# Performance work log

Hardware: AMD Instinct MI355X
Metric: run time of the kernel (lower is better)

Reference implementation:

```python
import math
import jax, jax.numpy as jnp
import numpy as np

HIDDEN = 1024
INTER = 2048
NUM_EXPERTS = 8          # includes 1 noop slot (last column)
TOP_K = 2
CAPACITY_FACTOR = 1.0
BATCH, SEQ = 4, 4096


def setup_inputs() -> dict:
    key = jax.random.key(0)
    k_x, k_rw, k_ei, k_eo = jax.random.split(key, 4)
    x = jax.random.normal(k_x, (BATCH, SEQ, HIDDEN), dtype=jnp.float32)
    # Router: nn.Linear(hidden, num_experts) with xavier_uniform weight, zero-ish bias
    limit = math.sqrt(6.0 / (HIDDEN + NUM_EXPERTS))
    router_w = jax.random.uniform(k_rw, (NUM_EXPERTS, HIDDEN), dtype=jnp.float32,
                                  minval=-limit, maxval=limit)
    router_b = jnp.zeros((NUM_EXPERTS,), dtype=jnp.float32)
    # Expert params initialized with randn, exactly as in the torch module
    experts_inter = jax.random.normal(k_ei, (NUM_EXPERTS - 1, HIDDEN, INTER), dtype=jnp.float32)
    experts_out = jax.random.normal(k_eo, (NUM_EXPERTS - 1, INTER, HIDDEN), dtype=jnp.float32)
    return {"x": x, "router_w": router_w, "router_b": router_b,
            "experts_inter": experts_inter, "experts_out": experts_out}


def reference(x, router_w, router_b, experts_inter, experts_out):
    B, S, H = x.shape
    E = router_w.shape[0]
    N = B * S
    capacity = math.ceil(N / E * CAPACITY_FACTOR)  # static (shapes are static)

    x_flat = x.reshape(N, H)
    # Router: linear + softmax over experts
    weights = jax.nn.softmax(x_flat @ router_w.T + router_b, axis=-1)   # [N, E]

    # Top-k sparsification: keep top-k weights per token, zero the rest
    vals, idx = jax.lax.top_k(weights, TOP_K)                            # [N, k]
    topk_w = jnp.zeros_like(weights).at[jnp.arange(N)[:, None], idx].set(vals)

    # Last expert column is the no-op (identity) path
    noop_routed = x_flat * topk_w[:, -1:]                                # [N, H]

    expert_w = topk_w[:, :-1]                                            # [N, E-1]
    mask = (expert_w > 0).astype(jnp.int32)                              # [N, E-1]

    # Per-expert: sort tokens by routing mask (descending), take first `capacity`
    sorted_idx = jnp.argsort(-mask, axis=0)[:capacity]                   # [C, E-1], stable
    sorted_mask = jnp.take_along_axis(mask, sorted_idx, axis=0)          # [C, E-1]

    used_idx = (sorted_idx * sorted_mask).reshape(-1)                    # [C*(E-1)]
    toks = x_flat[used_idx] * sorted_mask.reshape(-1)[:, None].astype(x.dtype)
    toks = toks.reshape(capacity, E - 1, H)                              # [C, E-1, H]
    in_w = jnp.take_along_axis(expert_w, sorted_idx, axis=0)             # [C, E-1]

    # Grouped expert FFN: relu(x W1) W2, weighted by routing prob
    h = jax.nn.relu(jnp.einsum('ceh,ehi->cei', toks, experts_inter))     # [C, E-1, I]
    out = jnp.einsum('cei,eih->ceh', h, experts_out) * in_w[..., None]   # [C, E-1, H]

    # Scatter-add combine (masked slots contribute zeros at index 0)
    combined = jnp.zeros_like(x_flat).at[used_idx].add(out.reshape(-1, H))
    combined = combined + noop_routed
    return combined.reshape(B, S, H)
```

## Files before the change

kernel.cpp:

```cpp
#include <hip/hip_runtime.h>
#include <stdint.h>

#define HIDDEN 1024
#define INTER 2048
#define NEXP 8
#define NE 7
#define NTOK 16384
#define CAP 2048
#define GBM 128
#define GBN 128

typedef __attribute__((ext_vector_type(8))) short short8;
typedef __attribute__((ext_vector_type(4))) float f32x4;

__device__ __forceinline__ unsigned short f2bf(float f) {
  union { float f; unsigned int u; } v;
  v.f = f;
  unsigned int u = v.u;
  unsigned int r = (u + 0x7FFFu + ((u >> 16) & 1u)) >> 16;
  return (unsigned short)r;
}

typedef __attribute__((address_space(1))) const unsigned int gu32;
typedef __attribute__((address_space(3))) unsigned int lu32;
__device__ __forceinline__ void gload16(const void* g, void* l) {
  __builtin_amdgcn_global_load_lds((gu32*)g, (lu32*)l, 16, 0, 0);
}

__global__ __launch_bounds__(256) void prologue_kernel(
    const float* __restrict__ x, const float* __restrict__ rw,
    const float* __restrict__ rb, float* __restrict__ expw,
    float* __restrict__ noopw, unsigned short* __restrict__ xbf,
    float* __restrict__ out, const float* __restrict__ wi,
    unsigned short* __restrict__ wiT) {
  int bx = blockIdx.x;
  int tid = threadIdx.x;
  if (bx > NTOK / 4) {
    int i = bx - (NTOK / 4 + 1);
    int e = i >> 9;
    int rem = i & 511;
    int k0 = (rem >> 5) * 64;
    int n0 = (rem & 31) * 64;
    const float* src = wi + (size_t)e * HIDDEN * INTER;
    unsigned short* dst = wiT + (size_t)e * HIDDEN * INTER;
    __shared__ float tile[64][65];
    int nr = tid & 15, kr = tid >> 4;
#pragma unroll
    for (int ii = 0; ii < 4; ii++) {
      int k = ii * 16 + kr;
      float4 v = *(const float4*)(src + (size_t)(k0 + k) * INTER + n0 + nr * 4);
      tile[k][nr * 4 + 0] = v.x;
      tile[k][nr * 4 + 1] = v.y;
      tile[k][nr * 4 + 2] = v.z;
      tile[k][nr * 4 + 3] = v.w;
    }
    __syncthreads();
    int g = tid & 7, nb = tid >> 3;
#pragma unroll
    for (int ii = 0; ii < 2; ii++) {
      int n = ii * 32 + nb;
      short8 p;
#pragma unroll
      for (int j = 0; j < 8; j++) p[j] = (short)f2bf(tile[g * 8 + j][n]);
      *(short8*)(dst + (size_t)(n0 + n) * HIDDEN + k0 + g * 8) = p;
    }
    return;
  }
  if (bx == NTOK / 4) {
    unsigned int* z = (unsigned int*)(xbf + (size_t)NTOK * HIDDEN);
    z[tid] = 0u;
    z[tid + 256] = 0u;
    return;
  }
  int wid = tid >> 6;
  int lane = tid & 63;
  int token = bx * 4 + wid;
  const float* xr = x + (size_t)token * HIDDEN;
  float4 xv[4];
  float acc[NEXP];
#pragma unroll
  for (int e = 0; e < NEXP; e++) acc[e] = 0.f;
#pragma unroll
  for (int j = 0; j < 4; j++) {
    xv[j] = *(const float4*)(xr + j * 256 + lane * 4);
#pragma unroll
    for (int e = 0; e < NEXP; e++) {
      float4 wv = *(const float4*)(rw + e * HIDDEN + j * 256 + lane * 4);
      acc[e] = fmaf(xv[j].x, wv.x, acc[e]);
      acc[e] = fmaf(xv[j].y, wv.y, acc[e]);
      acc[e] = fmaf(xv[j].z, wv.z, acc[e]);
      acc[e] = fmaf(xv[j].w, wv.w, acc[e]);
    }
  }
#pragma unroll
  for (int e = 0; e < NEXP; e++) {
    float a = acc[e];
#pragma unroll
    for (int off = 32; off > 0; off >>= 1) a += __shfl_xor(a, off);
    acc[e] = a + rb[e];
  }
  float nwv = 0.f;
  if (lane == 0) {
    float m = acc[0];
#pragma unroll
    for (int e = 1; e < NEXP; e++) m = fmaxf(m, acc[e]);
    float w[NEXP];
    float s = 0.f;
#pragma unroll
    for (int e = 0; e < NEXP; e++) { w[e] = expf(acc[e] - m); s += w[e]; }
    float inv = 1.f / s;
#pragma unroll
    for (int e = 0; e < NEXP; e++) w[e] *= inv;
    int t1 = 0;
#pragma unroll
    for (int e = 1; e < NEXP; e++) if (w[e] > w[t1]) t1 = e;
    int t2 = (t1 == 0) ? 1 : 0;
#pragma unroll
    for (int e = 0; e < NEXP; e++) if (e != t1 && w[e] > w[t2]) t2 = e;
    nwv = (t1 == NEXP - 1) ? w[t1] : ((t2 == NEXP - 1) ? w[t2] : 0.f);
    noopw[token] = nwv;
#pragma unroll
    for (int e = 0; e < NE; e++) {
      float v = 0.f;
      if (e == t1) v = w[e];
      if (e == t2) v = w[e];
      expw[(size_t)e * NTOK + token] = v;
    }
  }
  float nw = __shfl(nwv, 0);
  float* orow = out + (size_t)token * HIDDEN;
  unsigned short* brow = xbf + (size_t)token * HIDDEN;
#pragma unroll
  for (int j = 0; j < 4; j++) {
    float4 o = xv[j];
    o.x *= nw; o.y *= nw; o.z *= nw; o.w *= nw;
    *(float4*)(orow + j * 256 + lane * 4) = o;
    ushort4 b;
    b.x = f2bf(xv[j].x); b.y = f2bf(xv[j].y);
    b.z = f2bf(xv[j].z); b.w = f2bf(xv[j].w);
    *(ushort4*)(brow + j * 256 + lane * 4) = b;
  }
}

__global__ __launch_bounds__(1024) void assign_par_kernel(
    const float* __restrict__ expw, int* __restrict__ slot_tok,
    float* __restrict__ slot_w) {
  int e = blockIdx.x;
  int tid = threadIdx.x;
  int lane = tid & 63, w = tid >> 6;
  __shared__ int wtot[16];
  const float* we = expw + (size_t)e * NTOK;
  int base = 0;
#pragma unroll 1
  for (int r = 0; r < NTOK / 1024; r++) {
    int t = r * 1024 + tid;
    float wv = we[t];
    bool flag = wv > 0.f;
    unsigned long long mask = __ballot(flag);
    int lp = __popcll(mask & ((1ull << lane) - 1ull));
    if (lane == 0) wtot[w] = __popcll(mask);
    __syncthreads();
    int pre = 0, tot = 0;
#pragma unroll
    for (int i = 0; i < 16; i++) {
      int v = wtot[i];
      pre += (i < w) ? v : 0;
      tot += v;
    }
    int pos = base + pre + lp;
    if (flag && pos < CAP) {
      slot_tok[e * CAP + pos] = t;
      slot_w[e * CAP + pos] = wv;
    }
    base += tot;
    __syncthreads();
    if (base >= CAP) break;
  }
  int cnt = base < CAP ? base : CAP;
  for (int p = cnt + tid; p < CAP; p += 1024) {
    slot_tok[e * CAP + p] = -1;
    slot_w[e * CAP + p] = 0.f;
  }
}

__global__ __launch_bounds__(256) void transpose_bf16_kernel(
    const float* __restrict__ in, unsigned short* __restrict__ outp,
    int K, int N) {
  int e = blockIdx.z;
  const float* src = in + (size_t)e * K * N;
  unsigned short* dst = outp + (size_t)e * K * N;
  int k0 = blockIdx.y * 64;
  int n0 = blockIdx.x * 64;
  __shared__ float tile[64][65];
  int tid = threadIdx.x;
  int nr = tid & 15;
  int kr = tid >> 4;
#pragma unroll
  for (int i = 0; i < 4; i++) {
    int k = i * 16 + kr;
    float4 v = *(const float4*)(src + (size_t)(k0 + k) * N + n0 + nr * 4);
    tile[k][nr * 4 + 0] = v.x;
    tile[k][nr * 4 + 1] = v.y;
    tile[k][nr * 4 + 2] = v.z;
    tile[k][nr * 4 + 3] = v.w;
  }
  __syncthreads();
  int g = tid & 7;
  int nb = tid >> 3;
#pragma unroll
  for (int i = 0; i < 2; i++) {
    int n = i * 32 + nb;
    short8 p;
#pragma unroll
    for (int j = 0; j < 8; j++) p[j] = (short)f2bf(tile[g * 8 + j][n]);
    *(short8*)(dst + (size_t)(n0 + n) * K + k0 + g * 8) = p;
  }
}

__global__ __launch_bounds__(512, 4) void gemm1_mfma_kernel(
    const unsigned short* __restrict__ xbf, const unsigned short* __restrict__ wiT,
    const int* __restrict__ slot_tok, unsigned short* __restrict__ h,
    const float* __restrict__ wo, unsigned short* __restrict__ woT) {
  __shared__ __align__(16) unsigned short smem[GBM * 64 + GBN * 64];
  unsigned short* As = smem;
  unsigned short* Bs = smem + GBM * 64;
  int tid = threadIdx.x;
  if (blockIdx.y >= 16) {
    int e = blockIdx.z;
    int k0 = (blockIdx.y - 16) * 64;
    int n0 = blockIdx.x * 64;
    const float* src = wo + (size_t)e * INTER * HIDDEN;
    unsigned short* dst = woT + (size_t)e * INTER * HIDDEN;
    float* tile = (float*)smem;
    int nr = tid & 15, kr = tid >> 4;
#pragma unroll
    for (int ii = 0; ii < 2; ii++) {
      int k = ii * 32 + kr;
      float4 v = *(const float4*)(src + (size_t)(k0 + k) * HIDDEN + n0 + nr * 4);
      tile[k * 65 + nr * 4 + 0] = v.x;
      tile[k * 65 + nr * 4 + 1] = v.y;
      tile[k * 65 + nr * 4 + 2] = v.z;
      tile[k * 65 + nr * 4 + 3] = v.w;
    }
    __syncthreads();
    int g = tid & 7, n = tid >> 3;
    short8 p;
#pragma unroll
    for (int j = 0; j < 8; j++) p[j] = (short)f2bf(tile[(g * 8 + j) * 65 + n]);
    *(short8*)(dst + (size_t)(n0 + n) * INTER + k0 + g * 8) = p;
    return;
  }
  int orig = blockIdx.x + (blockIdx.y << 4) + (blockIdx.z << 8);
  int swz = (orig & 7) * 224 + (orig >> 3);
  int bxi = swz & 15, byi = (swz >> 4) & 15, bzi = swz >> 8;
  int e = bzi;
  const unsigned short* be = wiT + (size_t)e * HIDDEN * INTER;
  unsigned short* he = h + (size_t)e * CAP * INTER;
  int bm0 = byi * GBM;
  int bn0 = bxi * GBN;
  int lane = tid & 63, w = tid >> 6;
  int wm = w >> 2, wn = w & 3;

  const unsigned short* aptr[2];
  const unsigned short* bptr[2];
#pragma unroll
  for (int c = 0; c < 2; c++) {
    int slot = c * 512 + tid;
    int r = slot >> 3;
    int gb = slot & 7;
    int g = gb ^ (r & 7);
    int tok = slot_tok[e * CAP + bm0 + r];
    int row = tok < 0 ? NTOK : tok;
    aptr[c] = xbf + (size_t)row * HIDDEN + g * 8;
    bptr[c] = be + (size_t)(bn0 + r) * HIDDEN + g * 8;
  }

  f32x4 acc[4][2];
#pragma unroll
  for (int i = 0; i < 4; i++)
#pragma unroll
    for (int j = 0; j < 2; j++) acc[i][j] = (f32x4){0.f, 0.f, 0.f, 0.f};

  for (int k0 = 0; k0 < HIDDEN; k0 += 64) {
#pragma unroll
    for (int c = 0; c < 2; c++) {
      gload16(aptr[c] + k0, As + (c * 512 + tid) * 8);
      gload16(bptr[c] + k0, Bs + (c * 512 + tid) * 8);
    }
    __syncthreads();
#pragma unroll
    for (int kk = 0; kk < 2; kk++) {
      short8 a[4], b[2];
#pragma unroll
      for (int fm = 0; fm < 4; fm++) {
        int r = wm * 64 + fm * 16 + (lane & 15);
        int gb = (kk * 4 + (lane >> 4)) ^ (r & 7);
        a[fm] = *(const short8*)&As[r * 64 + gb * 8];
      }
#pragma unroll
      for (int fn = 0; fn < 2; fn++) {
        int n = wn * 32 + fn * 16 + (lane & 15);
        int gb = (kk * 4 + (lane >> 4)) ^ (n & 7);
        b[fn] = *(const short8*)&Bs[n * 64 + gb * 8];
      }
#pragma unroll
      for (int fm = 0; fm < 4; fm++)
#pragma unroll
        for (int fn = 0; fn < 2; fn++)
          acc[fm][fn] = __builtin_amdgcn_mfma_f32_16x16x32_bf16(
              a[fm], b[fn], acc[fm][fn], 0, 0, 0);
    }
    __syncthreads();
  }
#pragma unroll
  for (int fm = 0; fm < 4; fm++)
#pragma unroll
    for (int r4 = 0; r4 < 4; r4++) {
      int m = bm0 + wm * 64 + fm * 16 + ((lane >> 4) << 2) + r4;
#pragma unroll
      for (int fn = 0; fn < 2; fn++) {
        int n = bn0 + wn * 32 + fn * 16 + (lane & 15);
        float v = acc[fm][fn][r4];
        he[(size_t)m * INTER + n] = f2bf(v > 0.f ? v : 0.f);
      }
    }
}

__global__ __launch_bounds__(512, 4) void gemm2_mfma_kernel(
    const unsigned short* __restrict__ h, const unsigned short* __restrict__ woT,
    const int* __restrict__ slot_tok, const float* __restrict__ slot_w,
    float* __restrict__ out) {
  int orig = blockIdx.x + (blockIdx.y << 3) + (blockIdx.z << 7);
  int swz = (orig & 7) * 112 + (orig >> 3);
  int bxi = swz & 7, byi = (swz >> 3) & 15, bzi = swz >> 7;
  int e = bzi;
  const unsigned short* ae = h + (size_t)e * CAP * INTER;
  const unsigned short* be = woT + (size_t)e * INTER * HIDDEN;
  int bm0 = byi * GBM;
  int bn0 = bxi * GBN;
  __shared__ __align__(16) unsigned short smem[GBM * 64 + GBN * 64];
  unsigned short* As = smem;
  unsigned short* Bs = smem + GBM * 64;
  int tid = threadIdx.x;
  int lane = tid & 63, w = tid >> 6;
  int wm = w >> 2, wn = w & 3;

  const unsigned short* aptr[2];
  const unsigned short* bptr[2];
#pragma unroll
  for (int c = 0; c < 2; c++) {
    int slot = c * 512 + tid;
    int r = slot >> 3;
    int gb = slot & 7;
    int g = gb ^ (r & 7);
    aptr[c] = ae + (size_t)(bm0 + r) * INTER + g * 8;
    bptr[c] = be + (size_t)(bn0 + r) * INTER + g * 8;
  }

  f32x4 acc[4][2];
#pragma unroll
  for (int i = 0; i < 4; i++)
#pragma unroll
    for (int j = 0; j < 2; j++) acc[i][j] = (f32x4){0.f, 0.f, 0.f, 0.f};

  for (int k0 = 0; k0 < INTER; k0 += 64) {
#pragma unroll
    for (int c = 0; c < 2; c++) {
      gload16(aptr[c] + k0, As + (c * 512 + tid) * 8);
      gload16(bptr[c] + k0, Bs + (c * 512 + tid) * 8);
    }
    __syncthreads();
#pragma unroll
    for (int kk = 0; kk < 2; kk++) {
      short8 a[4], b[2];
#pragma unroll
      for (int fm = 0; fm < 4; fm++) {
        int r = wm * 64 + fm * 16 + (lane & 15);
        int gb = (kk * 4 + (lane >> 4)) ^ (r & 7);
        a[fm] = *(const short8*)&As[r * 64 + gb * 8];
      }
#pragma unroll
      for (int fn = 0; fn < 2; fn++) {
        int n = wn * 32 + fn * 16 + (lane & 15);
        int gb = (kk * 4 + (lane >> 4)) ^ (n & 7);
        b[fn] = *(const short8*)&Bs[n * 64 + gb * 8];
      }
#pragma unroll
      for (int fm = 0; fm < 4; fm++)
#pragma unroll
        for (int fn = 0; fn < 2; fn++)
          acc[fm][fn] = __builtin_amdgcn_mfma_f32_16x16x32_bf16(
              a[fm], b[fn], acc[fm][fn], 0, 0, 0);
    }
    __syncthreads();
  }
#pragma unroll
  for (int fm = 0; fm < 4; fm++)
#pragma unroll
    for (int r4 = 0; r4 < 4; r4++) {
      int m = bm0 + wm * 64 + fm * 16 + ((lane >> 4) << 2) + r4;
      int tok = slot_tok[e * CAP + m];
      float sw = slot_w[e * CAP + m];
      if (tok >= 0) {
#pragma unroll
        for (int fn = 0; fn < 2; fn++) {
          int n = bn0 + wn * 32 + fn * 16 + (lane & 15);
          unsafeAtomicAdd(out + (size_t)tok * HIDDEN + n, acc[fm][fn][r4] * sw);
        }
      }
    }
}

extern "C" void kernel_launch(void* const* d_in, const int* in_sizes, int n_in,
                              void* d_out, int out_size, void* d_ws, size_t ws_size,
                              hipStream_t stream) {
  const float* x = (const float*)d_in[0];
  const float* rw = (const float*)d_in[1];
  const float* rb = (const float*)d_in[2];
  const float* wi = (const float*)d_in[3];
  const float* wo = (const float*)d_in[4];
  float* out = (float*)d_out;
  char* ws = (char*)d_ws;

  const size_t h_bytes = (size_t)NE * CAP * INTER * 2;
  const size_t xbf_bytes = (size_t)(NTOK + 1) * HIDDEN * 2;
  const size_t wT_bytes = (size_t)NE * HIDDEN * INTER * 2;
  const size_t small_bytes = (size_t)NE * NTOK * 4 + (size_t)NTOK * 4 +
                             (size_t)NE * CAP * 4 * 2;
  const size_t need_mid = h_bytes + xbf_bytes + wT_bytes + small_bytes;
  const size_t need_full = need_mid + wT_bytes;

  bool fullp = ws_size >= need_full;
  unsigned short* h = (unsigned short*)ws;
  unsigned short* xbf = (unsigned short*)(ws + h_bytes);
  unsigned short* wiT = (unsigned short*)(ws + h_bytes + xbf_bytes);
  unsigned short* woT =
      fullp ? (unsigned short*)(ws + h_bytes + xbf_bytes + wT_bytes)
            : (unsigned short*)(ws + h_bytes);
  char* smalls = ws + (fullp ? need_full : need_mid) - small_bytes;
  float* expw = (float*)smalls;
  float* noopw = expw + (size_t)NE * NTOK;
  int* slot_tok = (int*)(noopw + NTOK);
  float* slot_w = (float*)(slot_tok + (size_t)NE * CAP);

  const int NPRO = NTOK / 4 + 1 + NE * 512;
  prologue_kernel<<<NPRO, 256, 0, stream>>>(x, rw, rb, expw, noopw, xbf, out,
                                            wi, wiT);
  assign_par_kernel<<<NE, 1024, 0, stream>>>(expw, slot_tok, slot_w);
  if (fullp) {
    gemm1_mfma_kernel<<<dim3(16, 48, NE), 512, 0, stream>>>(
        xbf, wiT, slot_tok, h, wo, woT);
  } else {
    gemm1_mfma_kernel<<<dim3(16, 16, NE), 512, 0, stream>>>(
        xbf, wiT, slot_tok, h, wo, woT);
    transpose_bf16_kernel<<<dim3(HIDDEN / 64, INTER / 64, NE), 256, 0, stream>>>(
        wo, woT, INTER, HIDDEN);
  }
  gemm2_mfma_kernel<<<dim3(8, 16, NE), 512, 0, stream>>>(
      h, woT, slot_tok, slot_w, out);
}
```

Baseline: 423.8 us.

## Double-buffer LDS tiles in both expert GEMMs to overlap loads with MFMA

Both grouped GEMM kernels now use two LDS buffers for A and B. The global-to-LDS loads for the next K tile are issued before the MFMA work on the current tile, with s_waitcnt vmcnt(4) so only the older loads must finish. The aim is to hide global memory latency behind matrix compute instead of stalling at each barrier. LDS use doubles to 64KB per block, which can lower occupancy below the requested 4 blocks per CU.

```diff
diff --git a/kernel.cpp b/kernel.cpp
--- a/kernel.cpp
+++ b/kernel.cpp
@@ -221,9 +221,8 @@
     const unsigned short* __restrict__ xbf, const unsigned short* __restrict__ wiT,
     const int* __restrict__ slot_tok, unsigned short* __restrict__ h,
     const float* __restrict__ wo, unsigned short* __restrict__ woT) {
-  __shared__ __align__(16) unsigned short smem[GBM * 64 + GBN * 64];
-  unsigned short* As = smem;
-  unsigned short* Bs = smem + GBM * 64;
+  __shared__ __align__(16) unsigned short As[2][GBM * 64];
+  __shared__ __align__(16) unsigned short Bs[2][GBN * 64];
   int tid = threadIdx.x;
   if (blockIdx.y >= 16) {
     int e = blockIdx.z;
@@ -231,7 +230,7 @@
     int n0 = blockIdx.x * 64;
     const float* src = wo + (size_t)e * INTER * HIDDEN;
     unsigned short* dst = woT + (size_t)e * INTER * HIDDEN;
-    float* tile = (float*)smem;
+    float* tile = (float*)As;
     int nr = tid & 15, kr = tid >> 4;
 #pragma unroll
     for (int ii = 0; ii < 2; ii++) {
@@ -281,13 +280,14 @@
 #pragma unroll
     for (int j = 0; j < 2; j++) acc[i][j] = (f32x4){0.f, 0.f, 0.f, 0.f};
 
-  for (int k0 = 0; k0 < HIDDEN; k0 += 64) {
+  auto stageT = [&](int k0, int buf) {
 #pragma unroll
     for (int c = 0; c < 2; c++) {
-      gload16(aptr[c] + k0, As + (c * 512 + tid) * 8);
-      gload16(bptr[c] + k0, Bs + (c * 512 + tid) * 8);
-    }
-    __syncthreads();
+      gload16(aptr[c] + k0, &As[buf][(c * 512 + tid) * 8]);
+      gload16(bptr[c] + k0, &Bs[buf][(c * 512 + tid) * 8]);
+    }
+  };
+  auto computeT = [&](int buf) {
 #pragma unroll
     for (int kk = 0; kk < 2; kk++) {
       short8 a[4], b[2];
@@ -295,13 +295,13 @@
       for (int fm = 0; fm < 4; fm++) {
         int r = wm * 64 + fm * 16 + (lane & 15);
         int gb = (kk * 4 + (lane >> 4)) ^ (r & 7);
-        a[fm] = *(const short8*)&As[r * 64 + gb * 8];
+        a[fm] = *(const short8*)&As[buf][r * 64 + gb * 8];
       }
 #pragma unroll
       for (int fn = 0; fn < 2; fn++) {
         int n = wn * 32 + fn * 16 + (lane & 15);
         int gb = (kk * 4 + (lane >> 4)) ^ (n & 7);
-        b[fn] = *(const short8*)&Bs[n * 64 + gb * 8];
+        b[fn] = *(const short8*)&Bs[buf][n * 64 + gb * 8];
       }
 #pragma unroll
       for (int fm = 0; fm < 4; fm++)
@@ -310,7 +310,23 @@
           acc[fm][fn] = __builtin_amdgcn_mfma_f32_16x16x32_bf16(
               a[fm], b[fn], acc[fm][fn], 0, 0, 0);
     }
-    __syncthreads();
+  };
+
+  const int nt = HIDDEN / 64;
+  stageT(0, 0);
+  int cur = 0;
+#pragma unroll 1
+  for (int t = 0; t < nt; t++) {
+    if (t + 1 < nt) {
+      stageT((t + 1) * 64, cur ^ 1);
+      asm volatile("s_waitcnt vmcnt(4)" ::: "memory");
+    } else {
+      asm volatile("s_waitcnt vmcnt(0)" ::: "memory");
+    }
+    __builtin_amdgcn_s_barrier();
+    computeT(cur);
+    __builtin_amdgcn_s_barrier();
+    cur ^= 1;
   }
 #pragma unroll
   for (int fm = 0; fm < 4; fm++)
@@ -338,9 +354,8 @@
   const unsigned short* be = woT + (size_t)e * INTER * HIDDEN;
   int bm0 = byi * GBM;
   int bn0 = bxi * GBN;
-  __shared__ __align__(16) unsigned short smem[GBM * 64 + GBN * 64];
-  unsigned short* As = smem;
-  unsigned short* Bs = smem + GBM * 64;
+  __shared__ __align__(16) unsigned short As[2][GBM * 64];
+  __shared__ __align__(16) unsigned short Bs[2][GBN * 64];
   int tid = threadIdx.x;
   int lane = tid & 63, w = tid >> 6;
   int wm = w >> 2, wn = w & 3;
@@ -363,13 +378,14 @@
 #pragma unroll
     for (int j = 0; j < 2; j++) acc[i][j] = (f32x4){0.f, 0.f, 0.f, 0.f};
 
-  for (int k0 = 0; k0 < INTER; k0 += 64) {
+  auto stageT = [&](int k0, int buf) {
 #pragma unroll
     for (int c = 0; c < 2; c++) {
-      gload16(aptr[c] + k0, As + (c * 512 + tid) * 8);
-      gload16(bptr[c] + k0, Bs + (c * 512 + tid) * 8);
-    }
-    __syncthreads();
+      gload16(aptr[c] + k0, &As[buf][(c * 512 + tid) * 8]);
+      gload16(bptr[c] + k0, &Bs[buf][(c * 512 + tid) * 8]);
+    }
+  };
+  auto computeT = [&](int buf) {
 #pragma unroll
     for (int kk = 0; kk < 2; kk++) {
       short8 a[4], b[2];
@@ -377,13 +393,13 @@
       for (int fm = 0; fm < 4; fm++) {
         int r = wm * 64 + fm * 16 + (lane & 15);
         int gb = (kk * 4 + (lane >> 4)) ^ (r & 7);
-        a[fm] = *(const short8*)&As[r * 64 + gb * 8];
+        a[fm] = *(const short8*)&As[buf][r * 64 + gb * 8];
       }
 #pragma unroll
       for (int fn = 0; fn < 2; fn++) {
         int n = wn * 32 + fn * 16 + (lane & 15);
         int gb = (kk * 4 + (lane >> 4)) ^ (n & 7);
-        b[fn] = *(const short8*)&Bs[n * 64 + gb * 8];
+        b[fn] = *(const short8*)&Bs[buf][n * 64 + gb * 8];
       }
 #pragma unroll
       for (int fm = 0; fm < 4; fm++)
@@ -392,7 +408,23 @@
           acc[fm][fn] = __builtin_amdgcn_mfma_f32_16x16x32_bf16(
               a[fm], b[fn], acc[fm][fn], 0, 0, 0);
     }
-    __syncthreads();
+  };
+
+  const int nt = INTER / 64;
+  stageT(0, 0);
+  int cur = 0;
+#pragma unroll 1
+  for (int t = 0; t < nt; t++) {
+    if (t + 1 < nt) {
+      stageT((t + 1) * 64, cur ^ 1);
+      asm volatile("s_waitcnt vmcnt(4)" ::: "memory");
+    } else {
+      asm volatile("s_waitcnt vmcnt(0)" ::: "memory");
+    }
+    __builtin_amdgcn_s_barrier();
+    computeT(cur);
+    __builtin_amdgcn_s_barrier();
+    cur ^= 1;
   }
 #pragma unroll
   for (int fm = 0; fm < 4; fm++)
```

New measurement: 410.6 us. -3.1%, faster.
